# Optimization experiments

Hardware: AMD Instinct MI355X
Metric: run time of the kernel (lower is better)

Reference implementation:

```python
import jax, jax.numpy as jnp
import numpy as np

N_NODES = 50000
N_EDGES = 600000
IN_DIM = 128
HID = 128
OUT_DIM = 40
NUM_REL = 3
LN_EPS = 1e-5


def layer_norm(x, g, b):
    mu = jnp.mean(x, axis=-1, keepdims=True)
    var = jnp.var(x, axis=-1, keepdims=True)
    return (x - mu) * jax.lax.rsqrt(var + LN_EPS) * g + b


def rgcn_conv(x, edge_index, edge_type, w_rel, w_root, bias, aggr):
    """PyG-style RGCNConv: out = x @ W_root + bias + sum_r aggr_r(x_src @ W_r)."""
    src, dst = edge_index[0], edge_index[1]
    out = x @ w_root + bias                      # [N, F_out]
    for r in range(NUM_REL):                     # small fixed relation loop
        h = x @ w_rel[r]                         # transform-then-gather: [N, F_out]
        msg = h[src]                             # [E, F_out]
        mask = (edge_type == r)[:, None]
        if aggr == 'add':
            msg = jnp.where(mask, msg, 0.0)
            agg = jax.ops.segment_sum(msg, dst, num_segments=N_NODES)
        else:  # 'max'; empty segments -> 0 (matches PyG scatter_reduce include_self=False over zeros)
            msg = jnp.where(mask, msg, -jnp.inf)
            agg = jax.ops.segment_max(msg, dst, num_segments=N_NODES)
            agg = jnp.where(jnp.isfinite(agg), agg, 0.0)
        out = out + agg
    return out


def setup_inputs() -> dict:
    key = jax.random.key(0)
    ks = jax.random.split(key, 16)
    f32 = jnp.float32
    def lin(k, fan_in, shape):
        return jax.random.normal(k, shape, dtype=f32) / np.sqrt(fan_in)
    inp = {
        'x': jax.random.normal(ks[0], (N_NODES, IN_DIM), dtype=f32),
        'edge_index': jax.random.randint(ks[1], (2, N_EDGES), 0, N_NODES),
        'edge_type': jax.random.randint(ks[2], (N_EDGES,), 0, NUM_REL),
        # conv1
        'w1_rel': lin(ks[3], IN_DIM, (NUM_REL, IN_DIM, HID)),
        'w1_root': lin(ks[4], IN_DIM, (IN_DIM, HID)),
        'b1': jnp.zeros((HID,), f32),
        'ln1_g': jnp.ones((HID,), f32), 'ln1_b': jnp.zeros((HID,), f32),
        # conv2
        'w2_rel': lin(ks[5], HID, (NUM_REL, HID, HID)),
        'w2_root': lin(ks[6], HID, (HID, HID)),
        'b2': jnp.zeros((HID,), f32),
        'ln2_g': jnp.ones((HID,), f32), 'ln2_b': jnp.zeros((HID,), f32),
        # classifier
        'cw1': lin(ks[7], HID, (HID, HID)), 'cb1': jnp.zeros((HID,), f32),
        'cln1_g': jnp.ones((HID,), f32), 'cln1_b': jnp.zeros((HID,), f32),
        'cw2': lin(ks[8], HID, (HID, HID // 2)), 'cb2': jnp.zeros((HID // 2,), f32),
        'cln2_g': jnp.ones((HID // 2,), f32), 'cln2_b': jnp.zeros((HID // 2,), f32),
        'cw3': lin(ks[9], HID // 2, (HID // 2, OUT_DIM)), 'cb3': jnp.zeros((OUT_DIM,), f32),
    }
    return inp


def reference(x, edge_index, edge_type,
              w1_rel, w1_root, b1, ln1_g, ln1_b,
              w2_rel, w2_root, b2, ln2_g, ln2_b,
              cw1, cb1, cln1_g, cln1_b,
              cw2, cb2, cln2_g, cln2_b,
              cw3, cb3):
    # eval mode: edge dropout and feature dropout are identity
    h = rgcn_conv(x, edge_index, edge_type, w1_rel, w1_root, b1, 'add')
    h = jax.nn.relu(layer_norm(h, ln1_g, ln1_b))
    x1 = h
    h = rgcn_conv(x1, edge_index, edge_type, w2_rel, w2_root, b2, 'max')
    h = jax.nn.relu(layer_norm(h, ln2_g, ln2_b))
    h = h + x1 * 0.2
    # classifier MLP
    h = jax.nn.gelu(layer_norm(h @ cw1 + cb1, cln1_g, cln1_b), approximate=False)
    h = jax.nn.gelu(layer_norm(h @ cw2 + cb2, cln2_g, cln2_b), approximate=False)
    h = h @ cw3 + cb3
    return jax.nn.log_softmax(h, axis=1)
```

## Files before the change

kernel.cpp:

```cpp
#include <hip/hip_runtime.h>
#include <hip/hip_bf16.h>
#include <math.h>


typedef __attribute__((ext_vector_type(8))) short bf16x8;
typedef __attribute__((ext_vector_type(4))) float f32x4;
typedef unsigned short ushort_t;

__device__ __forceinline__ ushort_t bf16rne(float v) {
    unsigned u = __float_as_uint(v);
    return (ushort_t)((u + 0x7FFFu + ((u >> 16) & 1u)) >> 16);
}

__device__ __forceinline__ void split_bf16(float v, ushort_t& h, ushort_t& l) {
    ushort_t hu = bf16rne(v);
    float hf = __uint_as_float((unsigned)hu << 16);
    float lo = v - hf;
    h = hu;
    l = bf16rne(lo);
}

__device__ __forceinline__ void split4(float4 v, uint2& h, uint2& l) {
    ushort_t h0, h1, h2, h3, l0, l1, l2, l3;
    split_bf16(v.x, h0, l0); split_bf16(v.y, h1, l1);
    split_bf16(v.z, h2, l2); split_bf16(v.w, h3, l3);
    h.x = (unsigned)h0 | ((unsigned)h1 << 16);
    h.y = (unsigned)h2 | ((unsigned)h3 << 16);
    l.x = (unsigned)l0 | ((unsigned)l1 << 16);
    l.y = (unsigned)l2 | ((unsigned)l3 << 16);
}

__device__ __forceinline__ float bf2f(unsigned u16) {
    return __uint_as_float(u16 << 16);
}

__device__ __forceinline__ float4 unpack_bf4(uint2 u) {
    return make_float4(bf2f(u.x & 0xFFFFu), bf2f(u.x >> 16),
                       bf2f(u.y & 0xFFFFu), bf2f(u.y >> 16));
}

__device__ __forceinline__ void conv_body128(const float* __restrict__ W,
                                             ushort_t* __restrict__ out,
                                             int idx) {
    constexpr int NCF = 8;
    constexpr size_t PST = (size_t)4 * NCF * 512;
    int l = idx & 63;
    int cf = (idx >> 6) & 7;
    int ks = idx >> 9;
    int col = cf * 16 + (l & 15);
    int k0 = ks * 32 + (l >> 4) * 8;
    size_t base = (((size_t)ks * NCF + cf) * 64 + l) * 8;
#pragma unroll
    for (int j = 0; j < 8; ++j) {
        ushort_t h, lo_;
        split_bf16(W[(size_t)(k0 + j) * 128 + col], h, lo_);
        out[base + j] = h;
        out[PST + base + j] = lo_;
    }
}

__global__ __launch_bounds__(256) void convert_all(
    const float* __restrict__ w1_root, const float* __restrict__ w1_rel,
    const float* __restrict__ w2_root, const float* __restrict__ w2_rel,
    const float* __restrict__ cw1, const float* __restrict__ cw2,
    ushort_t* __restrict__ wfb) {
    int b = blockIdx.x;
    if (b < 72) {
        const float* src;
        int slot;
        if (b < 8)       { slot = 0;               src = w1_root; }
        else if (b < 32) { int r = (b - 8) >> 3;   slot = 1 + r; src = w1_rel + (size_t)r * 16384; }
        else if (b < 40) { slot = 4;               src = w2_root; }
        else if (b < 64) { int r = (b - 40) >> 3;  slot = 5 + r; src = w2_rel + (size_t)r * 16384; }
        else             { slot = 8;               src = cw1; }
        int lb = (b < 8) ? b : (b < 32) ? ((b - 8) & 7) : (b < 40) ? (b - 32)
               : (b < 64) ? ((b - 40) & 7) : (b - 64);
        conv_body128(src, wfb + (size_t)slot * 32768, lb * 256 + threadIdx.x);
    } else {
        constexpr int NCF = 4;
        constexpr size_t PST = (size_t)4 * NCF * 512;
        int idx = (b - 72) * 256 + threadIdx.x;
        ushort_t* out = wfb + (size_t)9 * 32768;
        int l = idx & 63;
        int cf = (idx >> 6) & 3;
        int ks = idx >> 8;
        int col = cf * 16 + (l & 15);
        int k0 = ks * 32 + (l >> 4) * 8;
        size_t base = (((size_t)ks * NCF + cf) * 64 + l) * 8;
#pragma unroll
        for (int j = 0; j < 8; ++j) {
            ushort_t h, lo_;
            split_bf16(cw2[(size_t)(k0 + j) * 64 + col], h, lo_);
            out[base + j] = h;
            out[PST + base + j] = lo_;
        }
    }
}

__global__ __launch_bounds__(256) void x2bf(const float* __restrict__ x,
                                            ushort_t* __restrict__ xh, int n4) {
    int g = blockIdx.x * 256 + threadIdx.x;
    if (g >= n4) return;
    float4 v = ((const float4*)x)[g];
    uint2 o;
    o.x = (unsigned)bf16rne(v.x) | ((unsigned)bf16rne(v.y) << 16);
    o.y = (unsigned)bf16rne(v.z) | ((unsigned)bf16rne(v.w) << 16);
    ((uint2*)xh)[g] = o;
}

template <int NCOL, int NSEG, bool SPLIT0, int FUSE>
__global__ __launch_bounds__(256, 3) void gemm_planes(
    const char* __restrict__ A0, const char* __restrict__ A1,
    const char* __restrict__ A2, const char* __restrict__ A3,
    const ushort_t* __restrict__ wfrag, const float* __restrict__ bias,
    const float* __restrict__ lng, const float* __restrict__ lnb,
    void* __restrict__ Yv, int M) {
    constexpr int NCF = NCOL / 16;
    constexpr int WF = NCOL / 32;
    constexpr int PST = 4 * NCF * 512;
    constexpr int WSEG = 2 * PST;
    constexpr int RS = NCOL * 4 + 16;
    constexpr int EPB = 64 * RS;
    constexpr int SMEM_BYTES = (EPB > 32768) ? EPB : 32768;
    __shared__ __align__(16) char smem[SMEM_BYTES];
    char (*lds)[16384] = (char(*)[16384])smem;

    const int tid = threadIdx.x;
    const int wv = tid >> 6, lane = tid & 63, l15 = lane & 15, lg = lane >> 4;
    const int rowgrp = wv >> 1, colgrp = wv & 1;
    const int row0 = blockIdx.x * 64;
    const char* As[4] = {A0, A1, A2, A3};

    f32x4 acc[2][WF];
#pragma unroll
    for (int xf = 0; xf < 2; ++xf)
#pragma unroll
        for (int wf = 0; wf < WF; ++wf) acc[xf][wf] = (f32x4){0.f, 0.f, 0.f, 0.f};

    uint4 regs[4];

    auto LOADSTAGE = [&](int ch) {
        int seg = ch >> 1, kc = (ch & 1) * 64;
        const char* __restrict__ A = As[seg];
        if (SPLIT0 && seg == 0) {
#pragma unroll
            for (int i = 0; i < 4; ++i) {
                int s = tid + i * 256;
                int r = s >> 4, c4 = s & 15;
                int gr = row0 + r;
                float4 v = make_float4(0.f, 0.f, 0.f, 0.f);
                if (gr < M) v = *(const float4*)(A + (size_t)gr * 512 + kc * 4 + c4 * 16);
                regs[i] = *(uint4*)&v;
            }
        } else {
#pragma unroll
            for (int i = 0; i < 4; ++i) {
                int s = tid + i * 256;
                int p = s >> 9, r = (s >> 3) & 63, c16 = s & 7;
                int gr = row0 + r;
                uint4 v = make_uint4(0u, 0u, 0u, 0u);
                if (gr < M)
                    v = *(const uint4*)(A + (size_t)gr * 512 + p * 256 + kc * 2 + c16 * 16);
                regs[i] = v;
            }
        }
    };

    auto WRITESTAGE = [&](int ch, int buf) {
        char* L = lds[buf];
        if (SPLIT0 && (ch >> 1) == 0) {
#pragma unroll
            for (int i = 0; i < 4; ++i) {
                int s = tid + i * 256;
                int r = s >> 4, c4 = s & 15;
                uint2 hh, ll;
                float4 v = *(float4*)&regs[i];
                split4(v, hh, ll);
                int byte = (r * 128 + c4 * 8) ^ ((r & 7) << 4);
                *(uint2*)(L + byte) = hh;
                *(uint2*)(L + 8192 + byte) = ll;
            }
        } else {
#pragma unroll
            for (int i = 0; i < 4; ++i) {
                int s = tid + i * 256;
                int p = s >> 9, r = (s >> 3) & 63, c16 = s & 7;
                int byte = p * 8192 + ((r * 128 + c16 * 16) ^ ((r & 7) << 4));
                *(uint4*)(L + byte) = regs[i];
            }
        }
    };

    auto COMPUTE = [&](int ch, int buf) {
        int seg = ch >> 1, half = ch & 1;
        const ushort_t* __restrict__ ws = wfrag + (size_t)seg * WSEG;
        const char* L = lds[buf];
#pragma unroll
        for (int kk = 0; kk < 2; ++kk) {
            int ks = half * 2 + kk;
            bf16x8 xh[2], xl[2];
#pragma unroll
            for (int xf = 0; xf < 2; ++xf) {
                int r = rowgrp * 32 + xf * 16 + l15;
                int byte = (r * 128 + kk * 64 + lg * 16) ^ ((r & 7) << 4);
                xh[xf] = *(const bf16x8*)(L + byte);
                xl[xf] = *(const bf16x8*)(L + 8192 + byte);
            }
            bf16x8 wh[WF], wl[WF];
#pragma unroll
            for (int wf = 0; wf < WF; ++wf) {
                size_t off = (((size_t)ks * NCF + colgrp * WF + wf) * 64 + lane) * 8;
                wh[wf] = *(const bf16x8*)(ws + off);
                wl[wf] = *(const bf16x8*)(ws + PST + off);
            }
#pragma unroll
            for (int xf = 0; xf < 2; ++xf)
#pragma unroll
                for (int wf = 0; wf < WF; ++wf) {
                    acc[xf][wf] = __builtin_amdgcn_mfma_f32_16x16x32_bf16(
                        wh[wf], xh[xf], acc[xf][wf], 0, 0, 0);
                    acc[xf][wf] = __builtin_amdgcn_mfma_f32_16x16x32_bf16(
                        wl[wf], xh[xf], acc[xf][wf], 0, 0, 0);
                    acc[xf][wf] = __builtin_amdgcn_mfma_f32_16x16x32_bf16(
                        wh[wf], xl[xf], acc[xf][wf], 0, 0, 0);
                }
        }
    };

    constexpr int CH = 2 * NSEG;
    LOADSTAGE(0);
    WRITESTAGE(0, 0);
    __syncthreads();
    for (int ch = 0; ch < CH; ++ch) {
        if (ch + 1 < CH) LOADSTAGE(ch + 1);
        COMPUTE(ch, ch & 1);
        __syncthreads();
        if (ch + 1 < CH) WRITESTAGE(ch + 1, (ch + 1) & 1);
        __syncthreads();
    }

    {
        float4 bv[WF];
#pragma unroll
        for (int wf = 0; wf < WF; ++wf) {
            int col = colgrp * (NCOL / 2) + wf * 16 + lg * 4;
            bv[wf] = bias ? *(const float4*)(bias + col)
                          : make_float4(0.f, 0.f, 0.f, 0.f);
        }
#pragma unroll
        for (int xf = 0; xf < 2; ++xf) {
            int r = rowgrp * 32 + xf * 16 + l15;
#pragma unroll
            for (int wf = 0; wf < WF; ++wf) {
                int col = colgrp * (NCOL / 2) + wf * 16 + lg * 4;
                float4 o;
                o.x = acc[xf][wf][0] + bv[wf].x;
                o.y = acc[xf][wf][1] + bv[wf].y;
                o.z = acc[xf][wf][2] + bv[wf].z;
                o.w = acc[xf][wf][3] + bv[wf].w;
                *(float4*)(smem + r * RS + col * 4) = o;
            }
        }
    }
    __syncthreads();

    if (FUSE >= 1 && FUSE <= 3) {
        constexpr int CPT = NCOL / 4;
        int r = tid >> 2, seg = tid & 3;
        char* rp = smem + r * RS + seg * CPT * 4;
        float s = 0.f, sq = 0.f;
        float4 vv[CPT / 4];
#pragma unroll
        for (int j = 0; j < CPT / 4; ++j) {
            float4 v = *(const float4*)(rp + j * 16);
            vv[j] = v;
            s += (v.x + v.y) + (v.z + v.w);
            sq += (v.x * v.x + v.y * v.y) + (v.z * v.z + v.w * v.w);
        }
        s += __shfl_xor(s, 1, 64); sq += __shfl_xor(sq, 1, 64);
        s += __shfl_xor(s, 2, 64); sq += __shfl_xor(sq, 2, 64);
        float mu = s * (1.f / NCOL);
        float var = sq * (1.f / NCOL) - mu * mu;
        float rstd = rsqrtf(var + 1e-5f);
#pragma unroll
        for (int j = 0; j < CPT / 4; ++j) {
            int c0 = seg * CPT + j * 4;
            float4 v = vv[j];
            float4 gg = *(const float4*)(lng + c0);
            float4 bb = *(const float4*)(lnb + c0);
            float y0 = (v.x - mu) * rstd * gg.x + bb.x;
            float y1 = (v.y - mu) * rstd * gg.y + bb.y;
            float y2 = (v.z - mu) * rstd * gg.z + bb.z;
            float y3 = (v.w - mu) * rstd * gg.w + bb.w;
            if (FUSE == 1) {
                y0 = fmaxf(y0, 0.f); y1 = fmaxf(y1, 0.f);
                y2 = fmaxf(y2, 0.f); y3 = fmaxf(y3, 0.f);
            } else {
                y0 = 0.5f * y0 * (1.f + erff(y0 * 0.70710678118654752f));
                y1 = 0.5f * y1 * (1.f + erff(y1 * 0.70710678118654752f));
                y2 = 0.5f * y2 * (1.f + erff(y2 * 0.70710678118654752f));
                y3 = 0.5f * y3 * (1.f + erff(y3 * 0.70710678118654752f));
            }
            vv[j] = make_float4(y0, y1, y2, y3);
        }
        __syncthreads();
        if (FUSE == 3) {
#pragma unroll
            for (int j = 0; j < CPT / 4; ++j) *(float4*)(rp + j * 16) = vv[j];
        } else {
#pragma unroll
            for (int j = 0; j < CPT / 4; ++j) {
                int c0 = seg * CPT + j * 4;
                uint2 hw, lw;
                split4(vv[j], hw, lw);
                *(uint2*)(smem + r * RS + 2 * c0) = hw;
                *(uint2*)(smem + r * RS + 256 + 2 * c0) = lw;
            }
        }
        __syncthreads();
    }

    if (FUSE == 4) {
        constexpr int SL = 64 * 16;
#pragma unroll
        for (int i = 0; i < SL / 256; ++i) {
            int slot = tid + i * 256;
            int rr = slot >> 4, c16 = slot & 15;
            int gr = row0 + rr;
            if (gr < M) {
                float4 a = *(const float4*)(smem + rr * RS + c16 * 32);
                float4 b = *(const float4*)(smem + rr * RS + c16 * 32 + 16);
                uint4 o;
                o.x = (unsigned)bf16rne(a.x) | ((unsigned)bf16rne(a.y) << 16);
                o.y = (unsigned)bf16rne(a.z) | ((unsigned)bf16rne(a.w) << 16);
                o.z = (unsigned)bf16rne(b.x) | ((unsigned)bf16rne(b.y) << 16);
                o.w = (unsigned)bf16rne(b.z) | ((unsigned)bf16rne(b.w) << 16);
                *(uint4*)((char*)Yv + (size_t)gr * 256 + c16 * 16) = o;
            }
        }
    } else {
        constexpr int OUTB = (FUSE == 0 || FUSE == 3) ? NCOL * 4 : 512;
        constexpr int RP = OUTB / 16;
        constexpr int SL = 64 * RP;
#pragma unroll
        for (int i = 0; i < SL / 256; ++i) {
            int slot = tid + i * 256;
            int rr = slot / RP, c16 = slot % RP;
            int gr = row0 + rr;
            if (gr < M)
                *(uint4*)((char*)Yv + (size_t)gr * OUTB + c16 * 16) =
                    *(const uint4*)(smem + rr * RS + c16 * 16);
        }
    }
}

__global__ __launch_bounds__(256) void hist3_kernel(const int* __restrict__ edst,
                                                    const int* __restrict__ etype,
                                                    int* __restrict__ deg3, int E) {
    int e = blockIdx.x * 256 + threadIdx.x;
    if (e < E) atomicAdd(&deg3[edst[e] * 3 + etype[e]], 1);
}

__global__ __launch_bounds__(256) void degtot_kernel(const int* __restrict__ deg3,
                                                     int* __restrict__ degtot, int N) {
    int n = blockIdx.x * 256 + threadIdx.x;
    if (n < N) degtot[n] = deg3[n * 3] + deg3[n * 3 + 1] + deg3[n * 3 + 2];
}

__global__ __launch_bounds__(256) void scan_block(const int* __restrict__ in,
                                                  int* __restrict__ out,
                                                  int* __restrict__ sums, int n) {
    __shared__ int s[256];
    int g = blockIdx.x * 256 + threadIdx.x;
    int v = (g < n) ? in[g] : 0;
    s[threadIdx.x] = v;
    __syncthreads();
    int acc = v;
    for (int off = 1; off < 256; off <<= 1) {
        int t = (threadIdx.x >= off) ? s[threadIdx.x - off] : 0;
        __syncthreads();
        acc += t;
        s[threadIdx.x] = acc;
        __syncthreads();
    }
    if (g < n) out[g] = acc - v;
    if (threadIdx.x == 255 && sums) sums[blockIdx.x] = acc;
}

__global__ __launch_bounds__(256) void scan_add(int* __restrict__ out,
                                                const int* __restrict__ topex,
                                                int n, int total) {
    int g = blockIdx.x * 256 + threadIdx.x;
    if (g < n) out[g] += topex[blockIdx.x];
    if (g == 0) out[n] = total;
}

__global__ __launch_bounds__(256) void ranges_kernel(
    const int* __restrict__ rowptr, const int* __restrict__ deg3,
    int4* __restrict__ ranges, int* __restrict__ cursor3, int N) {
    int n = blockIdx.x * 256 + threadIdx.x;
    if (n >= N) return;
    int b = rowptr[n];
    int d0 = deg3[n * 3], d1 = deg3[n * 3 + 1];
    int4 r;
    r.x = b; r.y = b + d0; r.z = b + d0 + d1; r.w = rowptr[n + 1];
    ranges[n] = r;
    cursor3[n * 3] = r.x; cursor3[n * 3 + 1] = r.y; cursor3[n * 3 + 2] = r.z;
}

__global__ __launch_bounds__(256) void fill3_kernel(
    const int* __restrict__ esrc, const int* __restrict__ edst,
    const int* __restrict__ etype, int* __restrict__ cursor3,
    int* __restrict__ colidx, int E) {
    int e = blockIdx.x * 256 + threadIdx.x;
    if (e >= E) return;
    int pos = atomicAdd(&cursor3[edst[e] * 3 + etype[e]], 1);
    colidx[pos] = esrc[e];
}

__device__ __forceinline__ float4 gather_sum_bf(const ushort_t* __restrict__ XH,
                                                const int* __restrict__ colidx,
                                                int beg, int end, int l) {
    float4 a = make_float4(0.f, 0.f, 0.f, 0.f);
    int e = beg;
    for (; e + 4 <= end; e += 4) {
        int s0 = colidx[e], s1 = colidx[e + 1];
        int s2 = colidx[e + 2], s3 = colidx[e + 3];
        uint2 u0 = *(const uint2*)(XH + (size_t)s0 * 128 + l * 4);
        uint2 u1 = *(const uint2*)(XH + (size_t)s1 * 128 + l * 4);
        uint2 u2 = *(const uint2*)(XH + (size_t)s2 * 128 + l * 4);
        uint2 u3 = *(const uint2*)(XH + (size_t)s3 * 128 + l * 4);
        float4 v0 = unpack_bf4(u0), v1 = unpack_bf4(u1);
        float4 v2 = unpack_bf4(u2), v3 = unpack_bf4(u3);
        a.x += (v0.x + v1.x) + (v2.x + v3.x);
        a.y += (v0.y + v1.y) + (v2.y + v3.y);
        a.z += (v0.z + v1.z) + (v2.z + v3.z);
        a.w += (v0.w + v1.w) + (v2.w + v3.w);
    }
    for (; e < end; ++e) {
        float4 v = unpack_bf4(*(const uint2*)(XH + (size_t)colidx[e] * 128 + l * 4));
        a.x += v.x; a.y += v.y; a.z += v.z; a.w += v.w;
    }
    return a;
}

__device__ __forceinline__ void store_plane4(char* rowbase, int l, float4 a) {
    uint2 h, lo;
    split4(a, h, lo);
    *(uint2*)(rowbase + 8 * l) = h;
    *(uint2*)(rowbase + 256 + 8 * l) = lo;
}

__global__ __launch_bounds__(256) void agg3_add(
    const ushort_t* __restrict__ xh, const int4* __restrict__ ranges,
    const int* __restrict__ colidx, char* __restrict__ S0,
    char* __restrict__ S1, char* __restrict__ S2, int N) {
    int node = blockIdx.x * 8 + (threadIdx.x >> 5);
    int l = threadIdx.x & 31;
    if (node >= N) return;
    int4 rg = ranges[node];
    float4 a0 = gather_sum_bf(xh, colidx, rg.x, rg.y, l);
    float4 a1 = gather_sum_bf(xh, colidx, rg.y, rg.z, l);
    float4 a2 = gather_sum_bf(xh, colidx, rg.z, rg.w, l);
    store_plane4(S0 + (size_t)node * 512, l, a0);
    store_plane4(S1 + (size_t)node * 512, l, a1);
    store_plane4(S2 + (size_t)node * 512, l, a2);
}

__device__ __forceinline__ float4 gather_max_bf(const ushort_t* __restrict__ H,
                                                const int* __restrict__ colidx,
                                                int beg, int end, int l) {
    float4 m = make_float4(-INFINITY, -INFINITY, -INFINITY, -INFINITY);
    int e = beg;
    for (; e + 4 <= end; e += 4) {
        int s0 = colidx[e], s1 = colidx[e + 1];
        int s2 = colidx[e + 2], s3 = colidx[e + 3];
        float4 v0 = unpack_bf4(*(const uint2*)(H + (size_t)s0 * 128 + l * 4));
        float4 v1 = unpack_bf4(*(const uint2*)(H + (size_t)s1 * 128 + l * 4));
        float4 v2 = unpack_bf4(*(const uint2*)(H + (size_t)s2 * 128 + l * 4));
        float4 v3 = unpack_bf4(*(const uint2*)(H + (size_t)s3 * 128 + l * 4));
        m.x = fmaxf(m.x, fmaxf(fmaxf(v0.x, v1.x), fmaxf(v2.x, v3.x)));
        m.y = fmaxf(m.y, fmaxf(fmaxf(v0.y, v1.y), fmaxf(v2.y, v3.y)));
        m.z = fmaxf(m.z, fmaxf(fmaxf(v0.z, v1.z), fmaxf(v2.z, v3.z)));
        m.w = fmaxf(m.w, fmaxf(fmaxf(v0.w, v1.w), fmaxf(v2.w, v3.w)));
    }
    for (; e < end; ++e) {
        float4 v = unpack_bf4(*(const uint2*)(H + (size_t)colidx[e] * 128 + l * 4));
        m.x = fmaxf(m.x, v.x); m.y = fmaxf(m.y, v.y);
        m.z = fmaxf(m.z, v.z); m.w = fmaxf(m.w, v.w);
    }
    m.x = (m.x > -3e38f) ? m.x : 0.f;
    m.y = (m.y > -3e38f) ? m.y : 0.f;
    m.z = (m.z > -3e38f) ? m.z : 0.f;
    m.w = (m.w > -3e38f) ? m.w : 0.f;
    return m;
}

__global__ __launch_bounds__(256) void maxagg_ln(
    const ushort_t* __restrict__ H0, const ushort_t* __restrict__ H1,
    const ushort_t* __restrict__ H2, const int4* __restrict__ ranges,
    const int* __restrict__ colidx, const float* __restrict__ acc,
    const char* __restrict__ residP, const float* __restrict__ g,
    const float* __restrict__ b, char* __restrict__ outP, int N) {
    int node = blockIdx.x * 8 + (threadIdx.x >> 5);
    int l = threadIdx.x & 31;
    if (node >= N) return;
    int4 rg = ranges[node];
    float4 m0 = gather_max_bf(H0, colidx, rg.x, rg.y, l);
    float4 m1 = gather_max_bf(H1, colidx, rg.y, rg.z, l);
    float4 m2 = gather_max_bf(H2, colidx, rg.z, rg.w, l);
    float4 a = *(const float4*)(acc + (size_t)node * 128 + l * 4);
    a.x += m0.x + m1.x + m2.x;
    a.y += m0.y + m1.y + m2.y;
    a.z += m0.z + m1.z + m2.z;
    a.w += m0.w + m1.w + m2.w;
    float s = (a.x + a.y) + (a.z + a.w);
    float sq = (a.x * a.x + a.y * a.y) + (a.z * a.z + a.w * a.w);
#pragma unroll
    for (int off = 16; off; off >>= 1) {
        s += __shfl_xor(s, off, 64);
        sq += __shfl_xor(sq, off, 64);
    }
    float mu = s * (1.f / 128.f);
    float var = sq * (1.f / 128.f) - mu * mu;
    float rstd = rsqrtf(var + 1e-5f);
    float4 gg = *(const float4*)(g + l * 4);
    float4 bb = *(const float4*)(b + l * 4);
    float y0 = fmaxf((a.x - mu) * rstd * gg.x + bb.x, 0.f);
    float y1 = fmaxf((a.y - mu) * rstd * gg.y + bb.y, 0.f);
    float y2 = fmaxf((a.z - mu) * rstd * gg.z + bb.z, 0.f);
    float y3 = fmaxf((a.w - mu) * rstd * gg.w + bb.w, 0.f);
    const char* rb = residP + (size_t)node * 512;
    uint2 rh = *(const uint2*)(rb + 8 * l);
    uint2 rl = *(const uint2*)(rb + 256 + 8 * l);
    float4 rhi = unpack_bf4(rh), rlo = unpack_bf4(rl);
    y0 += 0.2f * (rhi.x + rlo.x);
    y1 += 0.2f * (rhi.y + rlo.y);
    y2 += 0.2f * (rhi.z + rlo.z);
    y3 += 0.2f * (rhi.w + rlo.w);
    store_plane4((char*)outP + (size_t)node * 512, l, make_float4(y0, y1, y2, y3));
}

__global__ __launch_bounds__(256) void gemm40_lsm(const float* __restrict__ X,
                                                  const float* __restrict__ W,
                                                  const float* __restrict__ bias,
                                                  float* __restrict__ Y, int M) {
    __shared__ float Xs[64][65];
    __shared__ float Ws[64 * 40];
    __shared__ float Ys[64][41];
    __shared__ float mx_[64], ls_[64];
    const int tid = threadIdx.x;
    const int row0 = blockIdx.x * 64;
    for (int i = tid; i < 64 * 40; i += 256) Ws[i] = W[i];
#pragma unroll
    for (int i = 0; i < 4; ++i) {
        int slot = tid + i * 256;
        int r = slot >> 4, c4 = slot & 15;
        float4 v = make_float4(0.f, 0.f, 0.f, 0.f);
        if (row0 + r < M) v = *(const float4*)(X + (size_t)(row0 + r) * 64 + c4 * 4);
        Xs[r][c4 * 4 + 0] = v.x; Xs[r][c4 * 4 + 1] = v.y;
        Xs[r][c4 * 4 + 2] = v.z; Xs[r][c4 * 4 + 3] = v.w;
    }
    __syncthreads();
    const int row = tid >> 2, cg = (tid & 3) * 10;
    float acc[10];
#pragma unroll
    for (int j = 0; j < 10; ++j) acc[j] = 0.f;
#pragma unroll 8
    for (int k = 0; k < 64; ++k) {
        float xv = Xs[row][k];
#pragma unroll
        for (int j = 0; j < 10; ++j) acc[j] = fmaf(xv, Ws[k * 40 + cg + j], acc[j]);
    }
#pragma unroll
    for (int j = 0; j < 10; ++j) Ys[row][cg + j] = acc[j] + bias[cg + j];
    __syncthreads();
    if (tid < 64) {
        float mx = -INFINITY;
#pragma unroll 8
        for (int c = 0; c < 40; ++c) mx = fmaxf(mx, Ys[tid][c]);
        float sum = 0.f;
#pragma unroll 8
        for (int c = 0; c < 40; ++c) sum += __expf(Ys[tid][c] - mx);
        mx_[tid] = mx;
        ls_[tid] = logf(sum);
    }
    __syncthreads();
#pragma unroll
    for (int i = 0; i < 10; ++i) {
        int slot = tid + i * 256;
        int r = slot / 40, c = slot % 40;
        int gr = row0 + r;
        if (gr < M) Y[(size_t)gr * 40 + c] = Ys[r][c] - mx_[r] - ls_[r];
    }
}

extern "C" void kernel_launch(void* const* d_in, const int* in_sizes, int n_in,
                              void* d_out, int out_size, void* d_ws, size_t ws_size,
                              hipStream_t stream) {
    const float* x       = (const float*)d_in[0];
    const int*   eidx    = (const int*)d_in[1];
    const int*   etype   = (const int*)d_in[2];
    const float* w1_rel  = (const float*)d_in[3];
    const float* w1_root = (const float*)d_in[4];
    const float* b1      = (const float*)d_in[5];
    const float* ln1_g   = (const float*)d_in[6];
    const float* ln1_b   = (const float*)d_in[7];
    const float* w2_rel  = (const float*)d_in[8];
    const float* w2_root = (const float*)d_in[9];
    const float* b2      = (const float*)d_in[10];
    const float* ln2_g   = (const float*)d_in[11];
    const float* ln2_b   = (const float*)d_in[12];
    const float* cw1     = (const float*)d_in[13];
    const float* cb1     = (const float*)d_in[14];
    const float* cln1_g  = (const float*)d_in[15];
    const float* cln1_b  = (const float*)d_in[16];
    const float* cw2     = (const float*)d_in[17];
    const float* cb2     = (const float*)d_in[18];
    const float* cln2_g  = (const float*)d_in[19];
    const float* cln2_b  = (const float*)d_in[20];
    const float* cw3     = (const float*)d_in[21];
    const float* cb3     = (const float*)d_in[22];

    const int N = in_sizes[0] / 128;
    const int E = in_sizes[1] / 2;
    const int* esrc = eidx;
    const int* edst = eidx + E;

    const size_t NFB = (size_t)N * 512;
    char* B0 = (char*)d_ws;
    char* B1 = B0 + NFB;
    char* B2 = B1 + NFB;
    char* B3 = B2 + NFB;

    int* rowptr  = (int*)B3;
    int* degtot  = rowptr + (N + 1);
    int* deg3    = degtot + N;
    int* cursor3 = deg3 + 3 * N;
    int* bsums   = cursor3 + 3 * N;
    int* btop    = bsums + 256;
    int4* ranges = (int4*)(((uintptr_t)(btop + 256) + 15) & ~(uintptr_t)15);
    int* colidx  = (int*)(ranges + N);
    ushort_t* wfb = (ushort_t*)(((uintptr_t)(colidx + E) + 255) & ~(uintptr_t)255);
    auto WSLOT = [&](int i) { return wfb + (size_t)i * 32768; };
    ushort_t* xh = (ushort_t*)(((uintptr_t)(wfb + 10 * 32768) + 255) & ~(uintptr_t)255);
    ushort_t* H0 = (ushort_t*)B2;
    ushort_t* H1 = (ushort_t*)(B2 + (size_t)N * 256);
    ushort_t* H2 = xh;

    const dim3 blk(256);
    const int gGemm = (N + 63) / 64;
    const int gAgg  = (N + 7) / 8;
    const int gEdge = (E + 255) / 256;
    const int gNode = (N + 255) / 256;
    const int nScanB = (N + 255) / 256;
    const int gX2  = (N * 32 + 255) / 256;

    hipMemsetAsync(deg3, 0, (size_t)3 * N * sizeof(int), stream);
    hist3_kernel<<<gEdge, blk, 0, stream>>>(edst, etype, deg3, E);
    degtot_kernel<<<gNode, blk, 0, stream>>>(deg3, degtot, N);
    scan_block<<<nScanB, blk, 0, stream>>>(degtot, rowptr, bsums, N);
    scan_block<<<1, blk, 0, stream>>>(bsums, btop, nullptr, nScanB);
    scan_add<<<nScanB, blk, 0, stream>>>(rowptr, btop, N, E);
    ranges_kernel<<<gNode, blk, 0, stream>>>(rowptr, deg3, ranges, cursor3, N);
    fill3_kernel<<<gEdge, blk, 0, stream>>>(esrc, edst, etype, cursor3, colidx, E);

    convert_all<<<76, blk, 0, stream>>>(w1_root, w1_rel, w2_root, w2_rel,
                                        cw1, cw2, wfb);
    x2bf<<<gX2, blk, 0, stream>>>(x, xh, N * 32);

    agg3_add<<<gAgg, blk, 0, stream>>>(xh, ranges, colidx, B0, B1, B2, N);
    gemm_planes<128, 4, true, 1><<<gGemm, blk, 0, stream>>>(
        (const char*)x, B0, B1, B2, WSLOT(0), b1, ln1_g, ln1_b, B0, N);

    gemm_planes<128, 1, false, 0><<<gGemm, blk, 0, stream>>>(
        B0, B0, B0, B0, WSLOT(4), b2, nullptr, nullptr, B1, N);
    gemm_planes<128, 1, false, 4><<<gGemm, blk, 0, stream>>>(
        B0, B0, B0, B0, WSLOT(5), nullptr, nullptr, nullptr, H0, N);
    gemm_planes<128, 1, false, 4><<<gGemm, blk, 0, stream>>>(
        B0, B0, B0, B0, WSLOT(6), nullptr, nullptr, nullptr, H1, N);
    gemm_planes<128, 1, false, 4><<<gGemm, blk, 0, stream>>>(
        B0, B0, B0, B0, WSLOT(7), nullptr, nullptr, nullptr, H2, N);
    maxagg_ln<<<gAgg, blk, 0, stream>>>(H0, H1, H2, ranges, colidx, (float*)B1,
                                        B0, ln2_g, ln2_b, B1, N);

    gemm_planes<128, 1, false, 2><<<gGemm, blk, 0, stream>>>(
        B1, B1, B1, B1, WSLOT(8), cb1, cln1_g, cln1_b, B0, N);
    gemm_planes<64, 1, false, 3><<<gGemm, blk, 0, stream>>>(
        B0, B0, B0, B0, WSLOT(9), cb2, cln2_g, cln2_b, B2, N);
    gemm40_lsm<<<gGemm, blk, 0, stream>>>((float*)B2, cw3, cb3, (float*)d_out, N);
}
```

Baseline: 311.8 us.

## Store activations as single bf16 plane and fuse conv2 GEMMs into one kernel

Activations move from a hi/lo split-bf16 layout (two planes, 512 bytes per row) to a single bf16 plane (256 bytes per row). This halves activation traffic in the GEMMs and aggregations and drops the third MFMA term (weight-hi × activation-lo). The four conv2 GEMMs (root and three relations) are merged into one kernel that loads the X tile into LDS once and loops over the weight sets. The trade-off is lower activation precision, since the first GEMM now reads bf16 x instead of the exact fp32 split, which could raise error against the reference.

```diff
diff --git a/kernel.cpp b/kernel.cpp
--- a/kernel.cpp
+++ b/kernel.cpp
@@ -15,19 +15,8 @@
 __device__ __forceinline__ void split_bf16(float v, ushort_t& h, ushort_t& l) {
     ushort_t hu = bf16rne(v);
     float hf = __uint_as_float((unsigned)hu << 16);
-    float lo = v - hf;
     h = hu;
-    l = bf16rne(lo);
-}
-
-__device__ __forceinline__ void split4(float4 v, uint2& h, uint2& l) {
-    ushort_t h0, h1, h2, h3, l0, l1, l2, l3;
-    split_bf16(v.x, h0, l0); split_bf16(v.y, h1, l1);
-    split_bf16(v.z, h2, l2); split_bf16(v.w, h3, l3);
-    h.x = (unsigned)h0 | ((unsigned)h1 << 16);
-    h.y = (unsigned)h2 | ((unsigned)h3 << 16);
-    l.x = (unsigned)l0 | ((unsigned)l1 << 16);
-    l.y = (unsigned)l2 | ((unsigned)l3 << 16);
+    l = bf16rne(v - hf);
 }
 
 __device__ __forceinline__ float bf2f(unsigned u16) {
@@ -37,6 +26,13 @@
 __device__ __forceinline__ float4 unpack_bf4(uint2 u) {
     return make_float4(bf2f(u.x & 0xFFFFu), bf2f(u.x >> 16),
                        bf2f(u.y & 0xFFFFu), bf2f(u.y >> 16));
+}
+
+__device__ __forceinline__ uint2 pack_bf4(float4 v) {
+    uint2 o;
+    o.x = (unsigned)bf16rne(v.x) | ((unsigned)bf16rne(v.y) << 16);
+    o.y = (unsigned)bf16rne(v.z) | ((unsigned)bf16rne(v.w) << 16);
+    return o;
 }
 
 __device__ __forceinline__ void conv_body128(const float* __restrict__ W,
@@ -68,11 +64,11 @@
     if (b < 72) {
         const float* src;
         int slot;
-        if (b < 8)       { slot = 0;               src = w1_root; }
-        else if (b < 32) { int r = (b - 8) >> 3;   slot = 1 + r; src = w1_rel + (size_t)r * 16384; }
-        else if (b < 40) { slot = 4;               src = w2_root; }
-        else if (b < 64) { int r = (b - 40) >> 3;  slot = 5 + r; src = w2_rel + (size_t)r * 16384; }
-        else             { slot = 8;               src = cw1; }
+        if (b < 8)       { slot = 0;              src = w1_root; }
+        else if (b < 32) { int r = (b - 8) >> 3;  slot = 1 + r; src = w1_rel + (size_t)r * 16384; }
+        else if (b < 40) { slot = 4;              src = w2_root; }
+        else if (b < 64) { int r = (b - 40) >> 3; slot = 5 + r; src = w2_rel + (size_t)r * 16384; }
+        else             { slot = 8;              src = cw1; }
         int lb = (b < 8) ? b : (b < 32) ? ((b - 8) & 7) : (b < 40) ? (b - 32)
                : (b < 64) ? ((b - 40) & 7) : (b - 64);
         conv_body128(src, wfb + (size_t)slot * 32768, lb * 256 + threadIdx.x);
@@ -102,16 +98,13 @@
     int g = blockIdx.x * 256 + threadIdx.x;
     if (g >= n4) return;
     float4 v = ((const float4*)x)[g];
-    uint2 o;
-    o.x = (unsigned)bf16rne(v.x) | ((unsigned)bf16rne(v.y) << 16);
-    o.y = (unsigned)bf16rne(v.z) | ((unsigned)bf16rne(v.w) << 16);
-    ((uint2*)xh)[g] = o;
-}
-
-template <int NCOL, int NSEG, bool SPLIT0, int FUSE>
-__global__ __launch_bounds__(256, 3) void gemm_planes(
-    const char* __restrict__ A0, const char* __restrict__ A1,
-    const char* __restrict__ A2, const char* __restrict__ A3,
+    ((uint2*)xh)[g] = pack_bf4(v);
+}
+
+template <int NCOL, int NSEG, int FUSE>
+__global__ __launch_bounds__(256, 3) void gemm_bf(
+    const ushort_t* __restrict__ A0, const ushort_t* __restrict__ A1,
+    const ushort_t* __restrict__ A2, const ushort_t* __restrict__ A3,
     const ushort_t* __restrict__ wfrag, const float* __restrict__ bias,
     const float* __restrict__ lng, const float* __restrict__ lnb,
     void* __restrict__ Yv, int M) {
@@ -121,15 +114,15 @@
     constexpr int WSEG = 2 * PST;
     constexpr int RS = NCOL * 4 + 16;
     constexpr int EPB = 64 * RS;
-    constexpr int SMEM_BYTES = (EPB > 32768) ? EPB : 32768;
+    constexpr int SMEM_BYTES = (EPB > 16384) ? EPB : 16384;
     __shared__ __align__(16) char smem[SMEM_BYTES];
-    char (*lds)[16384] = (char(*)[16384])smem;
+    char (*lds)[8192] = (char(*)[8192])smem;
 
     const int tid = threadIdx.x;
     const int wv = tid >> 6, lane = tid & 63, l15 = lane & 15, lg = lane >> 4;
     const int rowgrp = wv >> 1, colgrp = wv & 1;
     const int row0 = blockIdx.x * 64;
-    const char* As[4] = {A0, A1, A2, A3};
+    const ushort_t* As[4] = {A0, A1, A2, A3};
 
     f32x4 acc[2][WF];
 #pragma unroll
@@ -137,57 +130,31 @@
 #pragma unroll
         for (int wf = 0; wf < WF; ++wf) acc[xf][wf] = (f32x4){0.f, 0.f, 0.f, 0.f};
 
-    uint4 regs[4];
+    uint4 regs[2];
 
     auto LOADSTAGE = [&](int ch) {
-        int seg = ch >> 1, kc = (ch & 1) * 64;
-        const char* __restrict__ A = As[seg];
-        if (SPLIT0 && seg == 0) {
-#pragma unroll
-            for (int i = 0; i < 4; ++i) {
-                int s = tid + i * 256;
-                int r = s >> 4, c4 = s & 15;
-                int gr = row0 + r;
-                float4 v = make_float4(0.f, 0.f, 0.f, 0.f);
-                if (gr < M) v = *(const float4*)(A + (size_t)gr * 512 + kc * 4 + c4 * 16);
-                regs[i] = *(uint4*)&v;
-            }
-        } else {
-#pragma unroll
-            for (int i = 0; i < 4; ++i) {
-                int s = tid + i * 256;
-                int p = s >> 9, r = (s >> 3) & 63, c16 = s & 7;
-                int gr = row0 + r;
-                uint4 v = make_uint4(0u, 0u, 0u, 0u);
-                if (gr < M)
-                    v = *(const uint4*)(A + (size_t)gr * 512 + p * 256 + kc * 2 + c16 * 16);
-                regs[i] = v;
-            }
+        const ushort_t* __restrict__ A = As[ch >> 1];
+        int kcb = (ch & 1) * 128;
+#pragma unroll
+        for (int i = 0; i < 2; ++i) {
+            int s = tid + i * 256;
+            int r = s >> 3, c16 = s & 7;
+            int gr = row0 + r;
+            uint4 v = make_uint4(0u, 0u, 0u, 0u);
+            if (gr < M)
+                v = *(const uint4*)((const char*)A + (size_t)gr * 256 + kcb + c16 * 16);
+            regs[i] = v;
         }
     };
 
-    auto WRITESTAGE = [&](int ch, int buf) {
+    auto WRITESTAGE = [&](int buf) {
         char* L = lds[buf];
-        if (SPLIT0 && (ch >> 1) == 0) {
-#pragma unroll
-            for (int i = 0; i < 4; ++i) {
-                int s = tid + i * 256;
-                int r = s >> 4, c4 = s & 15;
-                uint2 hh, ll;
-                float4 v = *(float4*)&regs[i];
-                split4(v, hh, ll);
-                int byte = (r * 128 + c4 * 8) ^ ((r & 7) << 4);
-                *(uint2*)(L + byte) = hh;
-                *(uint2*)(L + 8192 + byte) = ll;
-            }
-        } else {
-#pragma unroll
-            for (int i = 0; i < 4; ++i) {
-                int s = tid + i * 256;
-                int p = s >> 9, r = (s >> 3) & 63, c16 = s & 7;
-                int byte = p * 8192 + ((r * 128 + c16 * 16) ^ ((r & 7) << 4));
-                *(uint4*)(L + byte) = regs[i];
-            }
+#pragma unroll
+        for (int i = 0; i < 2; ++i) {
+            int s = tid + i * 256;
+            int r = s >> 3, c16 = s & 7;
+            int byte = (r * 128 + c16 * 16) ^ ((r & 7) << 4);
+            *(uint4*)(L + byte) = regs[i];
         }
     };
 
@@ -198,13 +165,12 @@
 #pragma unroll
         for (int kk = 0; kk < 2; ++kk) {
             int ks = half * 2 + kk;
-            bf16x8 xh[2], xl[2];
+            bf16x8 xh[2];
 #pragma unroll
             for (int xf = 0; xf < 2; ++xf) {
                 int r = rowgrp * 32 + xf * 16 + l15;
                 int byte = (r * 128 + kk * 64 + lg * 16) ^ ((r & 7) << 4);
                 xh[xf] = *(const bf16x8*)(L + byte);
-                xl[xf] = *(const bf16x8*)(L + 8192 + byte);
             }
             bf16x8 wh[WF], wl[WF];
 #pragma unroll
@@ -221,21 +187,19 @@
                         wh[wf], xh[xf], acc[xf][wf], 0, 0, 0);
                     acc[xf][wf] = __builtin_amdgcn_mfma_f32_16x16x32_bf16(
                         wl[wf], xh[xf], acc[xf][wf], 0, 0, 0);
-                    acc[xf][wf] = __builtin_amdgcn_mfma_f32_16x16x32_bf16(
-                        wh[wf], xl[xf], acc[xf][wf], 0, 0, 0);
                 }
         }
     };
 
     constexpr int CH = 2 * NSEG;
     LOADSTAGE(0);
-    WRITESTAGE(0, 0);
+    WRITESTAGE(0);
     __syncthreads();
     for (int ch = 0; ch < CH; ++ch) {
         if (ch + 1 < CH) LOADSTAGE(ch + 1);
         COMPUTE(ch, ch & 1);
         __syncthreads();
-        if (ch + 1 < CH) WRITESTAGE(ch + 1, (ch + 1) & 1);
+        if (ch + 1 < CH) WRITESTAGE((ch + 1) & 1);
         __syncthreads();
     }
 
@@ -311,35 +275,30 @@
 #pragma unroll
             for (int j = 0; j < CPT / 4; ++j) {
                 int c0 = seg * CPT + j * 4;
-                uint2 hw, lw;
-                split4(vv[j], hw, lw);
-                *(uint2*)(smem + r * RS + 2 * c0) = hw;
-                *(uint2*)(smem + r * RS + 256 + 2 * c0) = lw;
+                *(uint2*)(smem + r * RS + 2 * c0) = pack_bf4(vv[j]);
             }
         }
         __syncthreads();
     }
 
     if (FUSE == 4) {
-        constexpr int SL = 64 * 16;
+        constexpr int SL = 64 * (NCOL / 8);
 #pragma unroll
         for (int i = 0; i < SL / 256; ++i) {
             int slot = tid + i * 256;
-            int rr = slot >> 4, c16 = slot & 15;
+            int rr = slot / (NCOL / 8), c16 = slot % (NCOL / 8);
             int gr = row0 + rr;
             if (gr < M) {
                 float4 a = *(const float4*)(smem + rr * RS + c16 * 32);
                 float4 b = *(const float4*)(smem + rr * RS + c16 * 32 + 16);
                 uint4 o;
-                o.x = (unsigned)bf16rne(a.x) | ((unsigned)bf16rne(a.y) << 16);
-                o.y = (unsigned)bf16rne(a.z) | ((unsigned)bf16rne(a.w) << 16);
-                o.z = (unsigned)bf16rne(b.x) | ((unsigned)bf16rne(b.y) << 16);
-                o.w = (unsigned)bf16rne(b.z) | ((unsigned)bf16rne(b.w) << 16);
-                *(uint4*)((char*)Yv + (size_t)gr * 256 + c16 * 16) = o;
+                uint2 pa = pack_bf4(a), pb = pack_bf4(b);
+                o.x = pa.x; o.y = pa.y; o.z = pb.x; o.w = pb.y;
+                *(uint4*)((char*)Yv + (size_t)gr * (NCOL * 2) + c16 * 16) = o;
             }
         }
     } else {
-        constexpr int OUTB = (FUSE == 0 || FUSE == 3) ? NCOL * 4 : 512;
+        constexpr int OUTB = (FUSE == 0 || FUSE == 3) ? NCOL * 4 : NCOL * 2;
         constexpr int RP = OUTB / 16;
         constexpr int SL = 64 * RP;
 #pragma unroll
@@ -350,6 +309,123 @@
             if (gr < M)
                 *(uint4*)((char*)Yv + (size_t)gr * OUTB + c16 * 16) =
                     *(const uint4*)(smem + rr * RS + c16 * 16);
+        }
+    }
+}
+
+__global__ __launch_bounds__(256, 3) void gemm_conv2(
+    const ushort_t* __restrict__ X, const ushort_t* __restrict__ wfb,
+    const float* __restrict__ b2, float* __restrict__ accOut,
+    ushort_t* __restrict__ H0, ushort_t* __restrict__ H1,
+    ushort_t* __restrict__ H2, int M) {
+    constexpr int NCF = 8, WF = 4;
+    constexpr int PST = 4 * NCF * 512;
+    constexpr int RS = 128 * 4 + 16;
+    __shared__ __align__(16) char smem[16384 + 64 * RS];
+    char* Xs = smem;
+    char* ep = smem + 16384;
+
+    const int tid = threadIdx.x;
+    const int wv = tid >> 6, lane = tid & 63, l15 = lane & 15, lg = lane >> 4;
+    const int rowgrp = wv >> 1, colgrp = wv & 1;
+    const int row0 = blockIdx.x * 64;
+
+#pragma unroll
+    for (int i = 0; i < 4; ++i) {
+        int s = tid + i * 256;
+        int r = s >> 4, c16 = s & 15;
+        int gr = row0 + r;
+        uint4 v = make_uint4(0u, 0u, 0u, 0u);
+        if (gr < M) v = *(const uint4*)((const char*)X + (size_t)gr * 256 + c16 * 16);
+        int byte = (r * 256 + c16 * 16) ^ ((r & 7) << 4);
+        *(uint4*)(Xs + byte) = v;
+    }
+    __syncthreads();
+
+    ushort_t* Hs[3] = {H0, H1, H2};
+    for (int set = 0; set < 4; ++set) {
+        const ushort_t* __restrict__ ws = wfb + (size_t)(4 + set) * 32768;
+        f32x4 acc[2][WF];
+#pragma unroll
+        for (int xf = 0; xf < 2; ++xf)
+#pragma unroll
+            for (int wf = 0; wf < WF; ++wf) acc[xf][wf] = (f32x4){0.f, 0.f, 0.f, 0.f};
+#pragma unroll
+        for (int ks = 0; ks < 4; ++ks) {
+            bf16x8 xh[2];
+#pragma unroll
+            for (int xf = 0; xf < 2; ++xf) {
+                int r = rowgrp * 32 + xf * 16 + l15;
+                int byte = (r * 256 + ks * 64 + lg * 16) ^ ((r & 7) << 4);
+                xh[xf] = *(const bf16x8*)(Xs + byte);
+            }
+            bf16x8 wh[WF], wl[WF];
+#pragma unroll
+            for (int wf = 0; wf < WF; ++wf) {
+                size_t off = (((size_t)ks * NCF + colgrp * WF + wf) * 64 + lane) * 8;
+                wh[wf] = *(const bf16x8*)(ws + off);
+                wl[wf] = *(const bf16x8*)(ws + PST + off);
+            }
+#pragma unroll
+            for (int xf = 0; xf < 2; ++xf)
+#pragma unroll
+                for (int wf = 0; wf < WF; ++wf) {
+                    acc[xf][wf] = __builtin_amdgcn_mfma_f32_16x16x32_bf16(
+                        wh[wf], xh[xf], acc[xf][wf], 0, 0, 0);
+                    acc[xf][wf] = __builtin_amdgcn_mfma_f32_16x16x32_bf16(
+                        wl[wf], xh[xf], acc[xf][wf], 0, 0, 0);
+                }
+        }
+        __syncthreads();
+        {
+            float4 bv[WF];
+#pragma unroll
+            for (int wf = 0; wf < WF; ++wf) {
+                int col = colgrp * 64 + wf * 16 + lg * 4;
+                bv[wf] = (set == 0) ? *(const float4*)(b2 + col)
+                                    : make_float4(0.f, 0.f, 0.f, 0.f);
+            }
+#pragma unroll
+            for (int xf = 0; xf < 2; ++xf) {
+                int r = rowgrp * 32 + xf * 16 + l15;
+#pragma unroll
+                for (int wf = 0; wf < WF; ++wf) {
+                    int col = colgrp * 64 + wf * 16 + lg * 4;
+                    float4 o;
+                    o.x = acc[xf][wf][0] + bv[wf].x;
+                    o.y = acc[xf][wf][1] + bv[wf].y;
+                    o.z = acc[xf][wf][2] + bv[wf].z;
+                    o.w = acc[xf][wf][3] + bv[wf].w;
+                    *(float4*)(ep + r * RS + col * 4) = o;
+                }
+            }
+        }
+        __syncthreads();
+        if (set == 0) {
+#pragma unroll
+            for (int i = 0; i < 8; ++i) {
+                int slot = tid + i * 256;
+                int rr = slot >> 5, c16 = slot & 31;
+                int gr = row0 + rr;
+                if (gr < M)
+                    *(uint4*)((char*)accOut + (size_t)gr * 512 + c16 * 16) =
+                        *(const uint4*)(ep + rr * RS + c16 * 16);
+            }
+        } else {
+            ushort_t* H = Hs[set - 1];
+#pragma unroll
+            for (int i = 0; i < 4; ++i) {
+                int slot = tid + i * 256;
+                int rr = slot >> 4, c16 = slot & 15;
+                int gr = row0 + rr;
+                if (gr < M) {
+                    float4 a = *(const float4*)(ep + rr * RS + c16 * 32);
+                    float4 b = *(const float4*)(ep + rr * RS + c16 * 32 + 16);
+                    uint2 pa = pack_bf4(a), pb = pack_bf4(b);
+                    uint4 o; o.x = pa.x; o.y = pa.y; o.z = pb.x; o.w = pb.y;
+                    *(uint4*)((char*)H + (size_t)gr * 256 + c16 * 16) = o;
+                }
+            }
         }
     }
 }
@@ -426,12 +502,10 @@
     for (; e + 4 <= end; e += 4) {
         int s0 = colidx[e], s1 = colidx[e + 1];
         int s2 = colidx[e + 2], s3 = colidx[e + 3];
-        uint2 u0 = *(const uint2*)(XH + (size_t)s0 * 128 + l * 4);
-        uint2 u1 = *(const uint2*)(XH + (size_t)s1 * 128 + l * 4);
-        uint2 u2 = *(const uint2*)(XH + (size_t)s2 * 128 + l * 4);
-        uint2 u3 = *(const uint2*)(XH + (size_t)s3 * 128 + l * 4);
-        float4 v0 = unpack_bf4(u0), v1 = unpack_bf4(u1);
-        float4 v2 = unpack_bf4(u2), v3 = unpack_bf4(u3);
+        float4 v0 = unpack_bf4(*(const uint2*)(XH + (size_t)s0 * 128 + l * 4));
+        float4 v1 = unpack_bf4(*(const uint2*)(XH + (size_t)s1 * 128 + l * 4));
+        float4 v2 = unpack_bf4(*(const uint2*)(XH + (size_t)s2 * 128 + l * 4));
+        float4 v3 = unpack_bf4(*(const uint2*)(XH + (size_t)s3 * 128 + l * 4));
         a.x += (v0.x + v1.x) + (v2.x + v3.x);
         a.y += (v0.y + v1.y) + (v2.y + v3.y);
         a.z += (v0.z + v1.z) + (v2.z + v3.z);
@@ -444,17 +518,10 @@
     return a;
 }
 
-__device__ __forceinline__ void store_plane4(char* rowbase, int l, float4 a) {
-    uint2 h, lo;
-    split4(a, h, lo);
-    *(uint2*)(rowbase + 8 * l) = h;
-    *(uint2*)(rowbase + 256 + 8 * l) = lo;
-}
-
 __global__ __launch_bounds__(256) void agg3_add(
     const ushort_t* __restrict__ xh, const int4* __restrict__ ranges,
-    const int* __restrict__ colidx, char* __restrict__ S0,
-    char* __restrict__ S1, char* __restrict__ S2, int N) {
+    const int* __restrict__ colidx, ushort_t* __restrict__ S0,
+    ushort_t* __restrict__ S1, ushort_t* __restrict__ S2, int N) {
     int node = blockIdx.x * 8 + (threadIdx.x >> 5);
     int l = threadIdx.x & 31;
     if (node >= N) return;
@@ -462,9 +529,9 @@
     float4 a0 = gather_sum_bf(xh, colidx, rg.x, rg.y, l);
     float4 a1 = gather_sum_bf(xh, colidx, rg.y, rg.z, l);
     float4 a2 = gather_sum_bf(xh, colidx, rg.z, rg.w, l);
-    store_plane4(S0 + (size_t)node * 512, l, a0);
-    store_plane4(S1 + (size_t)node * 512, l, a1);
-    store_plane4(S2 + (size_t)node * 512, l, a2);
+    *(uint2*)(S0 + (size_t)node * 128 + l * 4) = pack_bf4(a0);
+    *(uint2*)(S1 + (size_t)node * 128 + l * 4) = pack_bf4(a1);
+    *(uint2*)(S2 + (size_t)node * 128 + l * 4) = pack_bf4(a2);
 }
 
 __device__ __forceinline__ float4 gather_max_bf(const ushort_t* __restrict__ H,
@@ -500,8 +567,8 @@
     const ushort_t* __restrict__ H0, const ushort_t* __restrict__ H1,
     const ushort_t* __restrict__ H2, const int4* __restrict__ ranges,
     const int* __restrict__ colidx, const float* __restrict__ acc,
-    const char* __restrict__ residP, const float* __restrict__ g,
-    const float* __restrict__ b, char* __restrict__ outP, int N) {
+    const ushort_t* __restrict__ resid, const float* __restrict__ g,
+    const float* __restrict__ b, ushort_t* __restrict__ outH, int N) {
     int node = blockIdx.x * 8 + (threadIdx.x >> 5);
     int l = threadIdx.x & 31;
     if (node >= N) return;
@@ -526,19 +593,13 @@
     float rstd = rsqrtf(var + 1e-5f);
     float4 gg = *(const float4*)(g + l * 4);
     float4 bb = *(const float4*)(b + l * 4);
-    float y0 = fmaxf((a.x - mu) * rstd * gg.x + bb.x, 0.f);
-    float y1 = fmaxf((a.y - mu) * rstd * gg.y + bb.y, 0.f);
-    float y2 = fmaxf((a.z - mu) * rstd * gg.z + bb.z, 0.f);
-    float y3 = fmaxf((a.w - mu) * rstd * gg.w + bb.w, 0.f);
-    const char* rb = residP + (size_t)node * 512;
-    uint2 rh = *(const uint2*)(rb + 8 * l);
-    uint2 rl = *(const uint2*)(rb + 256 + 8 * l);
-    float4 rhi = unpack_bf4(rh), rlo = unpack_bf4(rl);
-    y0 += 0.2f * (rhi.x + rlo.x);
-    y1 += 0.2f * (rhi.y + rlo.y);
-    y2 += 0.2f * (rhi.z + rlo.z);
-    y3 += 0.2f * (rhi.w + rlo.w);
-    store_plane4((char*)outP + (size_t)node * 512, l, make_float4(y0, y1, y2, y3));
+    float4 rv = unpack_bf4(*(const uint2*)(resid + (size_t)node * 128 + l * 4));
+    float4 y;
+    y.x = fmaxf((a.x - mu) * rstd * gg.x + bb.x, 0.f) + 0.2f * rv.x;
+    y.y = fmaxf((a.y - mu) * rstd * gg.y + bb.y, 0.f) + 0.2f * rv.y;
+    y.z = fmaxf((a.z - mu) * rstd * gg.z + bb.z, 0.f) + 0.2f * rv.z;
+    y.w = fmaxf((a.w - mu) * rstd * gg.w + bb.w, 0.f) + 0.2f * rv.w;
+    *(uint2*)(outH + (size_t)node * 128 + l * 4) = pack_bf4(y);
 }
 
 __global__ __launch_bounds__(256) void gemm40_lsm(const float* __restrict__ X,
@@ -627,11 +688,14 @@
     const int* esrc = eidx;
     const int* edst = eidx + E;
 
-    const size_t NFB = (size_t)N * 512;
-    char* B0 = (char*)d_ws;
-    char* B1 = B0 + NFB;
-    char* B2 = B1 + NFB;
-    char* B3 = B2 + NFB;
+    const size_t HB = (size_t)N * 256;
+    char* base = (char*)d_ws;
+    ushort_t* S0 = (ushort_t*)(base + 0 * HB);
+    ushort_t* S1 = (ushort_t*)(base + 1 * HB);
+    ushort_t* S2 = (ushort_t*)(base + 2 * HB);
+    ushort_t* X1 = (ushort_t*)(base + 3 * HB);
+    float*    AC = (float*)   (base + 4 * HB);
+    char*     B3 = base + 6 * HB;
 
     int* rowptr  = (int*)B3;
     int* degtot  = rowptr + (N + 1);
@@ -644,9 +708,9 @@
     ushort_t* wfb = (ushort_t*)(((uintptr_t)(colidx + E) + 255) & ~(uintptr_t)255);
     auto WSLOT = [&](int i) { return wfb + (size_t)i * 32768; };
     ushort_t* xh = (ushort_t*)(((uintptr_t)(wfb + 10 * 32768) + 255) & ~(uintptr_t)255);
-    ushort_t* H0 = (ushort_t*)B2;
-    ushort_t* H1 = (ushort_t*)(B2 + (size_t)N * 256);
-    ushort_t* H2 = xh;
+    ushort_t* h2 = xh;
+    ushort_t* C1 = S0;
+    float*    C2 = (float*)S1;
 
     const dim3 blk(256);
     const int gGemm = (N + 63) / 64;
@@ -669,24 +733,17 @@
                                         cw1, cw2, wfb);
     x2bf<<<gX2, blk, 0, stream>>>(x, xh, N * 32);
 
-    agg3_add<<<gAgg, blk, 0, stream>>>(xh, ranges, colidx, B0, B1, B2, N);
-    gemm_planes<128, 4, true, 1><<<gGemm, blk, 0, stream>>>(
-        (const char*)x, B0, B1, B2, WSLOT(0), b1, ln1_g, ln1_b, B0, N);
-
-    gemm_planes<128, 1, false, 0><<<gGemm, blk, 0, stream>>>(
-        B0, B0, B0, B0, WSLOT(4), b2, nullptr, nullptr, B1, N);
-    gemm_planes<128, 1, false, 4><<<gGemm, blk, 0, stream>>>(
-        B0, B0, B0, B0, WSLOT(5), nullptr, nullptr, nullptr, H0, N);
-    gemm_planes<128, 1, false, 4><<<gGemm, blk, 0, stream>>>(
-        B0, B0, B0, B0, WSLOT(6), nullptr, nullptr, nullptr, H1, N);
-    gemm_planes<128, 1, false, 4><<<gGemm, blk, 0, stream>>>(
-        B0, B0, B0, B0, WSLOT(7), nullptr, nullptr, nullptr, H2, N);
-    maxagg_ln<<<gAgg, blk, 0, stream>>>(H0, H1, H2, ranges, colidx, (float*)B1,
-                                        B0, ln2_g, ln2_b, B1, N);
-
-    gemm_planes<128, 1, false, 2><<<gGemm, blk, 0, stream>>>(
-        B1, B1, B1, B1, WSLOT(8), cb1, cln1_g, cln1_b, B0, N);
-    gemm_planes<64, 1, false, 3><<<gGemm, blk, 0, stream>>>(
-        B0, B0, B0, B0, WSLOT(9), cb2, cln2_g, cln2_b, B2, N);
-    gemm40_lsm<<<gGemm, blk, 0, stream>>>((float*)B2, cw3, cb3, (float*)d_out, N);
-}
+    agg3_add<<<gAgg, blk, 0, stream>>>(xh, ranges, colidx, S0, S1, S2, N);
+    gemm_bf<128, 4, 1><<<gGemm, blk, 0, stream>>>(
+        xh, S0, S1, S2, WSLOT(0), b1, ln1_g, ln1_b, X1, N);
+
+    gemm_conv2<<<gGemm, blk, 0, stream>>>(X1, wfb, b2, AC, S0, S1, S2, N);
+    maxagg_ln<<<gAgg, blk, 0, stream>>>(S0, S1, S2, ranges, colidx, AC,
+                                        X1, ln2_g, ln2_b, h2, N);
+
+    gemm_bf<128, 1, 2><<<gGemm, blk, 0, stream>>>(
+        h2, h2, h2, h2, WSLOT(8), cb1, cln1_g, cln1_b, C1, N);
+    gemm_bf<64, 1, 3><<<gGemm, blk, 0, stream>>>(
+        C1, C1, C1, C1, WSLOT(9), cb2, cln2_g, cln2_b, C2, N);
+    gemm40_lsm<<<gGemm, blk, 0, stream>>>(C2, cw3, cb3, (float*)d_out, N);
+}
```

Measured after the change: 274.5 us. 12.0% less time.
